# Optimization experiments

Hardware: AMD Instinct MI355X
Metric: run time of the kernel (lower is better)

## Reference

```python
import jax, jax.numpy as jnp
import numpy as np

G, N, E, C = 4, 50000, 800000, 128


def setup_inputs() -> dict:
    key = jax.random.key(0)
    ks = jax.random.split(key, 8)
    x = jax.random.normal(ks[0], (G, N, C), dtype=jnp.float32)
    edge_index = jax.random.randint(ks[1], (G, 2, E), 0, N, dtype=jnp.int64)
    s = 1.0 / np.sqrt(C)
    W1 = jax.random.normal(ks[2], (G, C, C), dtype=jnp.float32) * s
    W2 = jax.random.normal(ks[3], (G, C, C), dtype=jnp.float32) * s
    W3 = jax.random.normal(ks[4], (G, C, C), dtype=jnp.float32) * s
    b1 = jnp.zeros((G, C), dtype=jnp.float32)
    b2 = jnp.zeros((G, C), dtype=jnp.float32)
    b3 = jnp.zeros((G, C), dtype=jnp.float32)
    return {"x": x, "edge_index": edge_index, "W1": W1, "b1": b1,
            "W2": W2, "b2": b2, "W3": W3, "b3": b3}


def _gcn_layer(x, src, dst, deg_inv_sqrt, W, b):
    # PyG GCNConv: linear, then D^-1/2 (A+I) D^-1/2 aggregation, then bias.
    h = x @ W                                   # [N, C_out]
    norm = deg_inv_sqrt[src] * deg_inv_sqrt[dst]  # [E+N]
    msg = h[src] * norm[:, None]                # gather + scale
    out = jax.ops.segment_sum(msg, dst, num_segments=x.shape[0])
    return out + b


def _forward_one(x, ei, W1, b1, W2, b2, W3, b3):
    n = x.shape[0]
    loops = jnp.arange(n, dtype=ei.dtype)
    src = jnp.concatenate([ei[0], loops])       # add self-loops
    dst = jnp.concatenate([ei[1], loops])
    deg = jax.ops.segment_sum(jnp.ones_like(src, dtype=x.dtype), dst, num_segments=n)
    dis = jnp.where(deg > 0, jax.lax.rsqrt(deg), 0.0)
    x = _gcn_layer(x, src, dst, dis, W1, b1)
    x = _gcn_layer(x, src, dst, dis, W2, b2)
    x = _gcn_layer(x, src, dst, dis, W3, b3)
    return x


def reference(x, edge_index, W1, b1, W2, b2, W3, b3):
    # vmap over the num_graphs independent GCN stacks, then concat node dim
    out = jax.vmap(_forward_one)(x, edge_index, W1, b1, W2, b2, W3, b3)
    return out.reshape(-1, out.shape[-1])       # [G*N, out_channels]
```

## Files before the change

kernel.cpp:

```cpp
#include <hip/hip_runtime.h>

#define NG 4
#define NN 50000
#define NE 800000
#define NC 128
#define NB 196
#define NBT (NG * NB)
#define CAPB 48
#define LBS (NB + 1)
#define CAPQ 4608

typedef _Float16 half8 __attribute__((ext_vector_type(8)));
typedef _Float16 half4 __attribute__((ext_vector_type(4)));
typedef float f32x4 __attribute__((ext_vector_type(4)));

__global__ __launch_bounds__(256) void init_cursors(int* __restrict__ bktCur) {
  int i = blockIdx.x * blockDim.x + threadIdx.x;
  if (i < NBT) bktCur[i] = i * CAPQ;
}

__global__ __launch_bounds__(256) void bucket_scatter(
    const int* __restrict__ ei, int* __restrict__ bktCur,
    unsigned int* __restrict__ rec) {
  __shared__ int lcnt[NB];
  __shared__ int lbase[NB];
  __shared__ unsigned int lbin[CAPB * LBS];
  int g = blockIdx.y;
  int tid = threadIdx.x;
  for (int i = tid; i < NB; i += 256) lcnt[i] = 0;
  __syncthreads();
  const int* srcp = ei + (size_t)g * 2 * NE;
  const int* dstp = srcp + NE;
  int e0 = blockIdx.x * 4096;
  for (int t = tid; t < 4096; t += 256) {
    int e = e0 + t;
    if (e < NE) {
      int s = srcp[e], d = dstp[e];
      int b = d >> 8;
      unsigned int r = ((unsigned int)(d & 255) << 16) | (unsigned int)s;
      int pos = atomicAdd(&lcnt[b], 1);
      if (pos < CAPB) lbin[pos * LBS + b] = r;
      else { int gp = atomicAdd(&bktCur[g * NB + b], 1); rec[gp] = r; }
    }
  }
  __syncthreads();
  if (tid < NB) {
    int n = lcnt[tid]; if (n > CAPB) n = CAPB;
    lbase[tid] = n ? atomicAdd(&bktCur[g * NB + tid], n) : 0;
  }
  __syncthreads();
  int lane = tid & 63, wv = tid >> 6;
  for (int b = wv; b < NB; b += 4) {
    int n = lcnt[b]; if (n > CAPB) n = CAPB;
    if (lane < n) rec[lbase[b] + lane] = lbin[lane * LBS + b];
  }
}

__global__ __launch_bounds__(256) void build_csr(
    const unsigned int* __restrict__ rec, const int* __restrict__ bktCur,
    unsigned short* __restrict__ col, int* __restrict__ off,
    unsigned short* __restrict__ deg, float* __restrict__ dis) {
  __shared__ int cnt[256];
  __shared__ int offv[256];
  __shared__ int cnt2[256];
  __shared__ int wsum[4];
  int g = blockIdx.y, b = blockIdx.x;
  int idx = g * NB + b;
  int rb = idx * CAPQ, re = bktCur[idx];
  int tid = threadIdx.x;
  cnt[tid] = 0;
  __syncthreads();
  for (int j = rb + tid; j < re; j += 256)
    atomicAdd(&cnt[(rec[j] >> 16) & 255], 1);
  __syncthreads();
  int lane = tid & 63, wv = tid >> 6;
  int v = cnt[tid], incl = v;
  #pragma unroll
  for (int d2 = 1; d2 < 64; d2 <<= 1) {
    int t = __shfl_up(incl, d2, 64);
    if (lane >= d2) incl += t;
  }
  if (lane == 63) wsum[wv] = incl;
  __syncthreads();
  if (tid == 0) {
    int s = 0;
    #pragma unroll
    for (int w = 0; w < 4; ++w) { int t = wsum[w]; wsum[w] = s; s += t; }
  }
  __syncthreads();
  int excl = wsum[wv] + incl - v;
  offv[tid] = excl;
  cnt2[tid] = 0;
  int node = b * 256 + tid;
  if (node < NN) {
    off[g * (NN + 1) + node] = rb + excl;
    deg[(size_t)g * NN + node] = (unsigned short)v;
    dis[(size_t)g * NN + node] = rsqrtf((float)(v + 1));
  }
  __syncthreads();
  for (int j = rb + tid; j < re; j += 256) {
    unsigned int r = rec[j];
    int dl = (r >> 16) & 255;
    int p = rb + offv[dl] + atomicAdd(&cnt2[dl], 1);
    col[p] = (unsigned short)(r & 0xFFFF);
  }
}

__global__ __launch_bounds__(256) void gemm_mfma_kernel(
    const float* __restrict__ x, const float* __restrict__ W,
    const float* __restrict__ dis, _Float16* __restrict__ h) {
  __shared__ _Float16 Wt[2][128 * 128];
  int g = blockIdx.y;
  int row0 = blockIdx.x * 128;
  int tid = threadIdx.x;
  int lane = tid & 63;
  int wv = tid >> 6;
  int kc = lane >> 4;
  int lr = lane & 15;
  const float* Wg = W + (size_t)g * NC * NC;
  const float* xg = x + (size_t)g * NN * NC;

  {
    int n = tid & 127;
    int kq = (tid >> 7) & 1;
    #pragma unroll
    for (int iter = 0; iter < 16; ++iter) {
      int k4 = iter * 8 + kq * 4;
      float w0 = Wg[(size_t)(k4 + 0) * NC + n];
      float w1 = Wg[(size_t)(k4 + 1) * NC + n];
      float w2 = Wg[(size_t)(k4 + 2) * NC + n];
      float w3 = Wg[(size_t)(k4 + 3) * NC + n];
      half4 hi, lo;
      hi[0] = (_Float16)w0; lo[0] = (_Float16)(w0 - (float)hi[0]);
      hi[1] = (_Float16)w1; lo[1] = (_Float16)(w1 - (float)hi[1]);
      hi[2] = (_Float16)w2; lo[2] = (_Float16)(w2 - (float)hi[2]);
      hi[3] = (_Float16)w3; lo[3] = (_Float16)(w3 - (float)hi[3]);
      int base = n * 128 + ((iter ^ (n & 15)) << 3) + kq * 4;
      *(half4*)&Wt[0][base] = hi;
      *(half4*)&Wt[1][base] = lo;
    }
  }
  __syncthreads();

  f32x4 acc[2][8];
  #pragma unroll
  for (int mb = 0; mb < 2; ++mb)
    #pragma unroll
    for (int nb = 0; nb < 8; ++nb)
      acc[mb][nb] = (f32x4){0.f, 0.f, 0.f, 0.f};

  for (int kstep = 0; kstep < 4; ++kstep) {
    half8 ah[2], al[2];
    #pragma unroll
    for (int mb = 0; mb < 2; ++mb) {
      int row = row0 + wv * 32 + mb * 16 + lr;
      if (row > NN - 1) row = NN - 1;
      const float* xp = xg + (size_t)row * NC + kstep * 32 + kc * 8;
      float4 v0 = *(const float4*)xp;
      float4 v1 = *(const float4*)(xp + 4);
      float vv0 = v0.x, vv1 = v0.y, vv2 = v0.z, vv3 = v0.w;
      float vv4 = v1.x, vv5 = v1.y, vv6 = v1.z, vv7 = v1.w;
      _Float16 t;
      t = (_Float16)vv0; ah[mb][0] = t; al[mb][0] = (_Float16)(vv0 - (float)t);
      t = (_Float16)vv1; ah[mb][1] = t; al[mb][1] = (_Float16)(vv1 - (float)t);
      t = (_Float16)vv2; ah[mb][2] = t; al[mb][2] = (_Float16)(vv2 - (float)t);
      t = (_Float16)vv3; ah[mb][3] = t; al[mb][3] = (_Float16)(vv3 - (float)t);
      t = (_Float16)vv4; ah[mb][4] = t; al[mb][4] = (_Float16)(vv4 - (float)t);
      t = (_Float16)vv5; ah[mb][5] = t; al[mb][5] = (_Float16)(vv5 - (float)t);
      t = (_Float16)vv6; ah[mb][6] = t; al[mb][6] = (_Float16)(vv6 - (float)t);
      t = (_Float16)vv7; ah[mb][7] = t; al[mb][7] = (_Float16)(vv7 - (float)t);
    }
    #pragma unroll
    for (int nb = 0; nb < 8; ++nb) {
      int n = nb * 16 + lr;
      int chunk = kstep * 4 + kc;
      int boff = n * 128 + ((chunk ^ (n & 15)) << 3);
      half8 bh = *(const half8*)&Wt[0][boff];
      half8 bl = *(const half8*)&Wt[1][boff];
      #pragma unroll
      for (int mb = 0; mb < 2; ++mb) {
        acc[mb][nb] = __builtin_amdgcn_mfma_f32_16x16x32_f16(ah[mb], bh, acc[mb][nb], 0, 0, 0);
        acc[mb][nb] = __builtin_amdgcn_mfma_f32_16x16x32_f16(al[mb], bh, acc[mb][nb], 0, 0, 0);
        acc[mb][nb] = __builtin_amdgcn_mfma_f32_16x16x32_f16(ah[mb], bl, acc[mb][nb], 0, 0, 0);
      }
    }
  }

  const float* disg = dis + (size_t)g * NN;
  _Float16* hg = h + (size_t)g * NN * NC;
  #pragma unroll
  for (int mb = 0; mb < 2; ++mb) {
    #pragma unroll
    for (int reg = 0; reg < 4; ++reg) {
      int row = row0 + wv * 32 + mb * 16 + kc * 4 + reg;
      if (row < NN) {
        float dsc = disg[row];
        half8 o;
        #pragma unroll
        for (int nb = 0; nb < 8; ++nb)
          o[nb] = (_Float16)(acc[mb][nb][reg] * dsc);
        *(half8*)(hg + (size_t)row * NC + lr * 8) = o;
      }
    }
  }
}

__global__ __launch_bounds__(256) void gemm16_mfma_kernel(
    const _Float16* __restrict__ x, const float* __restrict__ W,
    const float* __restrict__ dis, _Float16* __restrict__ h) {
  __shared__ _Float16 Wt[2][128 * 128];
  int g = blockIdx.y;
  int row0 = blockIdx.x * 128;
  int tid = threadIdx.x;
  int lane = tid & 63;
  int wv = tid >> 6;
  int kc = lane >> 4;
  int lr = lane & 15;
  const float* Wg = W + (size_t)g * NC * NC;
  const _Float16* xg = x + (size_t)g * NN * NC;

  {
    int n = tid & 127;
    int kq = (tid >> 7) & 1;
    #pragma unroll
    for (int iter = 0; iter < 16; ++iter) {
      int k4 = iter * 8 + kq * 4;
      float w0 = Wg[(size_t)(k4 + 0) * NC + n];
      float w1 = Wg[(size_t)(k4 + 1) * NC + n];
      float w2 = Wg[(size_t)(k4 + 2) * NC + n];
      float w3 = Wg[(size_t)(k4 + 3) * NC + n];
      half4 hi, lo;
      hi[0] = (_Float16)w0; lo[0] = (_Float16)(w0 - (float)hi[0]);
      hi[1] = (_Float16)w1; lo[1] = (_Float16)(w1 - (float)hi[1]);
      hi[2] = (_Float16)w2; lo[2] = (_Float16)(w2 - (float)hi[2]);
      hi[3] = (_Float16)w3; lo[3] = (_Float16)(w3 - (float)hi[3]);
      int base = n * 128 + ((iter ^ (n & 15)) << 3) + kq * 4;
      *(half4*)&Wt[0][base] = hi;
      *(half4*)&Wt[1][base] = lo;
    }
  }
  __syncthreads();

  f32x4 acc[2][8];
  #pragma unroll
  for (int mb = 0; mb < 2; ++mb)
    #pragma unroll
    for (int nb = 0; nb < 8; ++nb)
      acc[mb][nb] = (f32x4){0.f, 0.f, 0.f, 0.f};

  for (int kstep = 0; kstep < 4; ++kstep) {
    half8 ah[2];
    #pragma unroll
    for (int mb = 0; mb < 2; ++mb) {
      int row = row0 + wv * 32 + mb * 16 + lr;
      if (row > NN - 1) row = NN - 1;
      ah[mb] = *(const half8*)(xg + (size_t)row * NC + kstep * 32 + kc * 8);
    }
    #pragma unroll
    for (int nb = 0; nb < 8; ++nb) {
      int n = nb * 16 + lr;
      int chunk = kstep * 4 + kc;
      int boff = n * 128 + ((chunk ^ (n & 15)) << 3);
      half8 bh = *(const half8*)&Wt[0][boff];
      half8 bl = *(const half8*)&Wt[1][boff];
      #pragma unroll
      for (int mb = 0; mb < 2; ++mb) {
        acc[mb][nb] = __builtin_amdgcn_mfma_f32_16x16x32_f16(ah[mb], bh, acc[mb][nb], 0, 0, 0);
        acc[mb][nb] = __builtin_amdgcn_mfma_f32_16x16x32_f16(ah[mb], bl, acc[mb][nb], 0, 0, 0);
      }
    }
  }

  const float* disg = dis + (size_t)g * NN;
  _Float16* hg = h + (size_t)g * NN * NC;
  #pragma unroll
  for (int mb = 0; mb < 2; ++mb) {
    #pragma unroll
    for (int reg = 0; reg < 4; ++reg) {
      int row = row0 + wv * 32 + mb * 16 + kc * 4 + reg;
      if (row < NN) {
        float dsc = disg[row];
        half8 o;
        #pragma unroll
        for (int nb = 0; nb < 8; ++nb)
          o[nb] = (_Float16)(acc[mb][nb][reg] * dsc);
        *(half8*)(hg + (size_t)row * NC + lr * 8) = o;
      }
    }
  }
}

#define MIXACC(A, H) A = fmaf((float)(H), 1.0f, A)
template <bool F16OUT>
__global__ __launch_bounds__(256) void agg_kernel(
    const _Float16* __restrict__ h, const int* __restrict__ off,
    const unsigned short* __restrict__ col, const unsigned short* __restrict__ deg,
    const float* __restrict__ dis, const float* __restrict__ b,
    float* __restrict__ outf, _Float16* __restrict__ outh) {
  int bid = blockIdx.x;
  int g = (bid & 7) >> 1;
  int sub = ((bid >> 3) << 1) | (bid & 1);
  int node = sub * 16 + (threadIdx.x >> 4);
  if (sub >= NN / 16) return;
  int l = threadIdx.x & 15;
  const half8* h8 = (const half8*)(h + (size_t)g * NN * NC);
  float a0[8], a1[8], a2[8], a3[8];
  half8 v = h8[(size_t)node * 16 + l];
  #pragma unroll
  for (int i = 0; i < 8; ++i) {
    a0[i] = (float)v[i]; a1[i] = 0.f; a2[i] = 0.f; a3[i] = 0.f;
  }
  int s = off[g * (NN + 1) + node];
  int e = s + deg[(size_t)g * NN + node];
  int j = s;
  for (; j + 4 <= e; j += 4) {
    int c0 = col[j], c1 = col[j + 1], c2 = col[j + 2], c3 = col[j + 3];
    half8 v0 = h8[(size_t)c0 * 16 + l];
    half8 v1 = h8[(size_t)c1 * 16 + l];
    half8 v2 = h8[(size_t)c2 * 16 + l];
    half8 v3 = h8[(size_t)c3 * 16 + l];
    #pragma unroll
    for (int i = 0; i < 8; ++i) {
      MIXACC(a0[i], v0[i]); MIXACC(a1[i], v1[i]);
      MIXACC(a2[i], v2[i]); MIXACC(a3[i], v3[i]);
    }
  }
  for (; j < e; ++j) {
    half8 vr = h8[(size_t)col[j] * 16 + l];
    #pragma unroll
    for (int i = 0; i < 8; ++i) MIXACC(a0[i], vr[i]);
  }
  float dn = dis[g * NN + node];
  const float* bg = b + (size_t)g * NC;
  if constexpr (F16OUT) {
    _Float16* og = outh + ((size_t)g * NN + node) * NC;
    #pragma unroll
    for (int i = 0; i < 8; ++i) {
      float val = (a0[i] + a1[i] + a2[i] + a3[i]) * dn + bg[i * 16 + l];
      og[i * 16 + l] = (_Float16)val;
    }
  } else {
    float* og = outf + ((size_t)g * NN + node) * NC;
    #pragma unroll
    for (int i = 0; i < 8; ++i) {
      float val = (a0[i] + a1[i] + a2[i] + a3[i]) * dn + bg[i * 16 + l];
      og[i * 16 + l] = val;
    }
  }
}

extern "C" void kernel_launch(void* const* d_in, const int* in_sizes, int n_in,
                              void* d_out, int out_size, void* d_ws, size_t ws_size,
                              hipStream_t stream) {
  const float* x  = (const float*)d_in[0];
  const int*   ei = (const int*)d_in[1];
  const float* W1 = (const float*)d_in[2];
  const float* b1 = (const float*)d_in[3];
  const float* W2 = (const float*)d_in[4];
  const float* b2 = (const float*)d_in[5];
  const float* W3 = (const float*)d_in[6];
  const float* b3 = (const float*)d_in[7];
  float* out = (float*)d_out;

  char* ws = (char*)d_ws;
  size_t p = 0;
  auto carve = [&](size_t bytes) -> char* {
    char* r = ws + p;
    p += (bytes + 255) & ~(size_t)255;
    return r;
  };
  int*            bktCur = (int*)           carve((size_t)NBT * 4);
  unsigned short* col    = (unsigned short*)carve((size_t)NBT * CAPQ * 2);
  int*            off    = (int*)           carve((size_t)NG * (NN + 1) * 4);
  unsigned short* deg    = (unsigned short*)carve((size_t)NG * NN * 2);
  float*          dis    = (float*)         carve((size_t)NG * NN * 4);
  _Float16*       hbuf   = (_Float16*)      carve((size_t)NG * NN * NC * 2);
  size_t ubytes = (size_t)NG * NN * NC * 2;
  char*           uni    = carve(ubytes);
  unsigned int*   rec    = (unsigned int*)uni;
  _Float16*       xh     = (_Float16*)uni;

  init_cursors<<<(NBT + 255) / 256, 256, 0, stream>>>(bktCur);
  bucket_scatter<<<dim3((NE + 4095) / 4096, NG), 256, 0, stream>>>(ei, bktCur, rec);
  build_csr<<<dim3(NB, NG), 256, 0, stream>>>(rec, bktCur, col, off, deg, dis);

  dim3 ggrid((NN + 127) / 128, NG);
  int  agrid = ((NN / 16 + 1) / 2) * 8;

  gemm_mfma_kernel<<<ggrid, 256, 0, stream>>>(x, W1, dis, hbuf);
  agg_kernel<true><<<agrid, 256, 0, stream>>>(hbuf, off, col, deg, dis, b1, nullptr, xh);
  gemm16_mfma_kernel<<<ggrid, 256, 0, stream>>>(xh, W2, dis, hbuf);
  agg_kernel<true><<<agrid, 256, 0, stream>>>(hbuf, off, col, deg, dis, b2, nullptr, xh);
  gemm16_mfma_kernel<<<ggrid, 256, 0, stream>>>(xh, W3, dis, hbuf);
  agg_kernel<false><<<agrid, 256, 0, stream>>>(hbuf, off, col, deg, dis, b3, out, nullptr);
}
```

Before: 459.8 us.

## Fuse first-layer GEMM with edge bucket scatter in one heterogeneous launch

The first GEMM no longer depends on the degree normalisation. It now runs in the same launch as the edge bucket scatter, with blocks split by index, so the compute-bound MFMA work overlaps the atomic-heavy scatter. The source-side deg^-1/2 scaling for layer 1 moves into the aggregation kernel as a per-neighbour gather of dis. The layer-2/3 GEMM now uses 512-thread blocks covering 256 rows. This costs extra per-edge dis loads in the first aggregation and larger blocks with 64KB of shared memory.

```diff
diff --git a/kernel.cpp b/kernel.cpp
--- a/kernel.cpp
+++ b/kernel.cpp
@@ -9,6 +9,7 @@
 #define CAPB 48
 #define LBS (NB + 1)
 #define CAPQ 4608
+#define GEMM_BLKS 784
 
 typedef _Float16 half8 __attribute__((ext_vector_type(8)));
 typedef _Float16 half4 __attribute__((ext_vector_type(4)));
@@ -19,40 +20,131 @@
   if (i < NBT) bktCur[i] = i * CAPQ;
 }
 
-__global__ __launch_bounds__(256) void bucket_scatter(
-    const int* __restrict__ ei, int* __restrict__ bktCur,
-    unsigned int* __restrict__ rec) {
-  __shared__ int lcnt[NB];
-  __shared__ int lbase[NB];
-  __shared__ unsigned int lbin[CAPB * LBS];
-  int g = blockIdx.y;
+__global__ __launch_bounds__(512) void fat_gemm1_scatter(
+    const float* __restrict__ x, const float* __restrict__ W,
+    _Float16* __restrict__ h, const int* __restrict__ ei,
+    int* __restrict__ bktCur, unsigned int* __restrict__ rec) {
+  __shared__ char smem[65536];
+  int bid = blockIdx.x;
   int tid = threadIdx.x;
-  for (int i = tid; i < NB; i += 256) lcnt[i] = 0;
-  __syncthreads();
-  const int* srcp = ei + (size_t)g * 2 * NE;
-  const int* dstp = srcp + NE;
-  int e0 = blockIdx.x * 4096;
-  for (int t = tid; t < 4096; t += 256) {
-    int e = e0 + t;
-    if (e < NE) {
-      int s = srcp[e], d = dstp[e];
-      int b = d >> 8;
-      unsigned int r = ((unsigned int)(d & 255) << 16) | (unsigned int)s;
-      int pos = atomicAdd(&lcnt[b], 1);
-      if (pos < CAPB) lbin[pos * LBS + b] = r;
-      else { int gp = atomicAdd(&bktCur[g * NB + b], 1); rec[gp] = r; }
-    }
-  }
-  __syncthreads();
-  if (tid < NB) {
-    int n = lcnt[tid]; if (n > CAPB) n = CAPB;
-    lbase[tid] = n ? atomicAdd(&bktCur[g * NB + tid], n) : 0;
-  }
-  __syncthreads();
-  int lane = tid & 63, wv = tid >> 6;
-  for (int b = wv; b < NB; b += 4) {
-    int n = lcnt[b]; if (n > CAPB) n = CAPB;
-    if (lane < n) rec[lbase[b] + lane] = lbin[lane * LBS + b];
+  if (bid < GEMM_BLKS) {
+    _Float16* Wt0 = (_Float16*)smem;
+    _Float16* Wt1 = Wt0 + 128 * 128;
+    int g = bid / 196;
+    int row0 = (bid % 196) * 256;
+    int lane = tid & 63;
+    int wv = tid >> 6;
+    int kc = lane >> 4;
+    int lr = lane & 15;
+    const float* Wg = W + (size_t)g * NC * NC;
+    const float* xg = x + (size_t)g * NN * NC;
+    {
+      int n = tid & 127;
+      int kq = (tid >> 7) & 3;
+      #pragma unroll
+      for (int it = 0; it < 8; ++it) {
+        int k4 = it * 16 + kq * 4;
+        float w0 = Wg[(size_t)(k4 + 0) * NC + n];
+        float w1 = Wg[(size_t)(k4 + 1) * NC + n];
+        float w2 = Wg[(size_t)(k4 + 2) * NC + n];
+        float w3 = Wg[(size_t)(k4 + 3) * NC + n];
+        half4 hi, lo;
+        hi[0] = (_Float16)w0; lo[0] = (_Float16)(w0 - (float)hi[0]);
+        hi[1] = (_Float16)w1; lo[1] = (_Float16)(w1 - (float)hi[1]);
+        hi[2] = (_Float16)w2; lo[2] = (_Float16)(w2 - (float)hi[2]);
+        hi[3] = (_Float16)w3; lo[3] = (_Float16)(w3 - (float)hi[3]);
+        int chunk = k4 >> 3;
+        int base = n * 128 + ((chunk ^ (n & 15)) << 3) + (k4 & 4);
+        *(half4*)&Wt0[base] = hi;
+        *(half4*)&Wt1[base] = lo;
+      }
+    }
+    __syncthreads();
+    f32x4 acc[2][8];
+    #pragma unroll
+    for (int mb = 0; mb < 2; ++mb)
+      #pragma unroll
+      for (int nb = 0; nb < 8; ++nb)
+        acc[mb][nb] = (f32x4){0.f, 0.f, 0.f, 0.f};
+    for (int kstep = 0; kstep < 4; ++kstep) {
+      half8 ah[2], al[2];
+      #pragma unroll
+      for (int mb = 0; mb < 2; ++mb) {
+        int row = row0 + wv * 32 + mb * 16 + lr;
+        if (row > NN - 1) row = NN - 1;
+        const float* xp = xg + (size_t)row * NC + kstep * 32 + kc * 8;
+        float4 v0 = *(const float4*)xp;
+        float4 v1 = *(const float4*)(xp + 4);
+        float vv[8] = {v0.x, v0.y, v0.z, v0.w, v1.x, v1.y, v1.z, v1.w};
+        #pragma unroll
+        for (int i = 0; i < 8; ++i) {
+          _Float16 t = (_Float16)vv[i];
+          ah[mb][i] = t; al[mb][i] = (_Float16)(vv[i] - (float)t);
+        }
+      }
+      #pragma unroll
+      for (int nb = 0; nb < 8; ++nb) {
+        int n = nb * 16 + lr;
+        int chunk = kstep * 4 + kc;
+        int boff = n * 128 + ((chunk ^ (n & 15)) << 3);
+        half8 bh = *(const half8*)&Wt0[boff];
+        half8 bl = *(const half8*)&Wt1[boff];
+        #pragma unroll
+        for (int mb = 0; mb < 2; ++mb) {
+          acc[mb][nb] = __builtin_amdgcn_mfma_f32_16x16x32_f16(ah[mb], bh, acc[mb][nb], 0, 0, 0);
+          acc[mb][nb] = __builtin_amdgcn_mfma_f32_16x16x32_f16(al[mb], bh, acc[mb][nb], 0, 0, 0);
+          acc[mb][nb] = __builtin_amdgcn_mfma_f32_16x16x32_f16(ah[mb], bl, acc[mb][nb], 0, 0, 0);
+        }
+      }
+    }
+    _Float16* hg = h + (size_t)g * NN * NC;
+    #pragma unroll
+    for (int mb = 0; mb < 2; ++mb) {
+      #pragma unroll
+      for (int reg = 0; reg < 4; ++reg) {
+        int row = row0 + wv * 32 + mb * 16 + kc * 4 + reg;
+        if (row < NN) {
+          half8 o;
+          #pragma unroll
+          for (int nb = 0; nb < 8; ++nb)
+            o[nb] = (_Float16)acc[mb][nb][reg];
+          *(half8*)(hg + (size_t)row * NC + lr * 8) = o;
+        }
+      }
+    }
+  } else {
+    int* lcnt = (int*)smem;
+    int* lbase = lcnt + NB;
+    unsigned int* lbin = (unsigned int*)(smem + 2048);
+    int sb = bid - GEMM_BLKS;
+    int g = sb / 196;
+    int e0 = (sb % 196) * 4096;
+    for (int i = tid; i < NB; i += 512) lcnt[i] = 0;
+    __syncthreads();
+    const int* srcp = ei + (size_t)g * 2 * NE;
+    const int* dstp = srcp + NE;
+    for (int t = tid; t < 4096; t += 512) {
+      int e = e0 + t;
+      if (e < NE) {
+        int s = srcp[e], d = dstp[e];
+        int b = d >> 8;
+        unsigned int r = ((unsigned int)(d & 255) << 16) | (unsigned int)s;
+        int pos = atomicAdd(&lcnt[b], 1);
+        if (pos < CAPB) lbin[pos * LBS + b] = r;
+        else { int gp = atomicAdd(&bktCur[g * NB + b], 1); rec[gp] = r; }
+      }
+    }
+    __syncthreads();
+    if (tid < NB) {
+      int n = lcnt[tid]; if (n > CAPB) n = CAPB;
+      lbase[tid] = n ? atomicAdd(&bktCur[g * NB + tid], n) : 0;
+    }
+    __syncthreads();
+    int lane = tid & 63, wv = tid >> 6;
+    for (int b = wv; b < NB; b += 8) {
+      int n = lcnt[b]; if (n > CAPB) n = CAPB;
+      if (lane < n) rec[lbase[b] + lane] = lbin[lane * LBS + b];
+    }
   }
 }
 
@@ -106,26 +198,25 @@
   }
 }
 
-__global__ __launch_bounds__(256) void gemm_mfma_kernel(
-    const float* __restrict__ x, const float* __restrict__ W,
+__global__ __launch_bounds__(512) void gemm16_mfma_kernel(
+    const _Float16* __restrict__ x, const float* __restrict__ W,
     const float* __restrict__ dis, _Float16* __restrict__ h) {
   __shared__ _Float16 Wt[2][128 * 128];
   int g = blockIdx.y;
-  int row0 = blockIdx.x * 128;
+  int row0 = blockIdx.x * 256;
   int tid = threadIdx.x;
   int lane = tid & 63;
   int wv = tid >> 6;
   int kc = lane >> 4;
   int lr = lane & 15;
   const float* Wg = W + (size_t)g * NC * NC;
-  const float* xg = x + (size_t)g * NN * NC;
-
+  const _Float16* xg = x + (size_t)g * NN * NC;
   {
     int n = tid & 127;
-    int kq = (tid >> 7) & 1;
-    #pragma unroll
-    for (int iter = 0; iter < 16; ++iter) {
-      int k4 = iter * 8 + kq * 4;
+    int kq = (tid >> 7) & 3;
+    #pragma unroll
+    for (int it = 0; it < 8; ++it) {
+      int k4 = it * 16 + kq * 4;
       float w0 = Wg[(size_t)(k4 + 0) * NC + n];
       float w1 = Wg[(size_t)(k4 + 1) * NC + n];
       float w2 = Wg[(size_t)(k4 + 2) * NC + n];
@@ -135,40 +226,26 @@
       hi[1] = (_Float16)w1; lo[1] = (_Float16)(w1 - (float)hi[1]);
       hi[2] = (_Float16)w2; lo[2] = (_Float16)(w2 - (float)hi[2]);
       hi[3] = (_Float16)w3; lo[3] = (_Float16)(w3 - (float)hi[3]);
-      int base = n * 128 + ((iter ^ (n & 15)) << 3) + kq * 4;
+      int chunk = k4 >> 3;
+      int base = n * 128 + ((chunk ^ (n & 15)) << 3) + (k4 & 4);
       *(half4*)&Wt[0][base] = hi;
       *(half4*)&Wt[1][base] = lo;
     }
   }
   __syncthreads();
-
   f32x4 acc[2][8];
   #pragma unroll
   for (int mb = 0; mb < 2; ++mb)
     #pragma unroll
     for (int nb = 0; nb < 8; ++nb)
       acc[mb][nb] = (f32x4){0.f, 0.f, 0.f, 0.f};
-
   for (int kstep = 0; kstep < 4; ++kstep) {
-    half8 ah[2], al[2];
+    half8 ah[2];
     #pragma unroll
     for (int mb = 0; mb < 2; ++mb) {
       int row = row0 + wv * 32 + mb * 16 + lr;
       if (row > NN - 1) row = NN - 1;
-      const float* xp = xg + (size_t)row * NC + kstep * 32 + kc * 8;
-      float4 v0 = *(const float4*)xp;
-      float4 v1 = *(const float4*)(xp + 4);
-      float vv0 = v0.x, vv1 = v0.y, vv2 = v0.z, vv3 = v0.w;
-      float vv4 = v1.x, vv5 = v1.y, vv6 = v1.z, vv7 = v1.w;
-      _Float16 t;
-      t = (_Float16)vv0; ah[mb][0] = t; al[mb][0] = (_Float16)(vv0 - (float)t);
-      t = (_Float16)vv1; ah[mb][1] = t; al[mb][1] = (_Float16)(vv1 - (float)t);
-      t = (_Float16)vv2; ah[mb][2] = t; al[mb][2] = (_Float16)(vv2 - (float)t);
-      t = (_Float16)vv3; ah[mb][3] = t; al[mb][3] = (_Float16)(vv3 - (float)t);
-      t = (_Float16)vv4; ah[mb][4] = t; al[mb][4] = (_Float16)(vv4 - (float)t);
-      t = (_Float16)vv5; ah[mb][5] = t; al[mb][5] = (_Float16)(vv5 - (float)t);
-      t = (_Float16)vv6; ah[mb][6] = t; al[mb][6] = (_Float16)(vv6 - (float)t);
-      t = (_Float16)vv7; ah[mb][7] = t; al[mb][7] = (_Float16)(vv7 - (float)t);
+      ah[mb] = *(const half8*)(xg + (size_t)row * NC + kstep * 32 + kc * 8);
     }
     #pragma unroll
     for (int nb = 0; nb < 8; ++nb) {
@@ -180,12 +257,10 @@
       #pragma unroll
       for (int mb = 0; mb < 2; ++mb) {
         acc[mb][nb] = __builtin_amdgcn_mfma_f32_16x16x32_f16(ah[mb], bh, acc[mb][nb], 0, 0, 0);
-        acc[mb][nb] = __builtin_amdgcn_mfma_f32_16x16x32_f16(al[mb], bh, acc[mb][nb], 0, 0, 0);
         acc[mb][nb] = __builtin_amdgcn_mfma_f32_16x16x32_f16(ah[mb], bl, acc[mb][nb], 0, 0, 0);
       }
     }
   }
-
   const float* disg = dis + (size_t)g * NN;
   _Float16* hg = h + (size_t)g * NN * NC;
   #pragma unroll
@@ -205,93 +280,9 @@
   }
 }
 
-__global__ __launch_bounds__(256) void gemm16_mfma_kernel(
-    const _Float16* __restrict__ x, const float* __restrict__ W,
-    const float* __restrict__ dis, _Float16* __restrict__ h) {
-  __shared__ _Float16 Wt[2][128 * 128];
-  int g = blockIdx.y;
-  int row0 = blockIdx.x * 128;
-  int tid = threadIdx.x;
-  int lane = tid & 63;
-  int wv = tid >> 6;
-  int kc = lane >> 4;
-  int lr = lane & 15;
-  const float* Wg = W + (size_t)g * NC * NC;
-  const _Float16* xg = x + (size_t)g * NN * NC;
-
-  {
-    int n = tid & 127;
-    int kq = (tid >> 7) & 1;
-    #pragma unroll
-    for (int iter = 0; iter < 16; ++iter) {
-      int k4 = iter * 8 + kq * 4;
-      float w0 = Wg[(size_t)(k4 + 0) * NC + n];
-      float w1 = Wg[(size_t)(k4 + 1) * NC + n];
-      float w2 = Wg[(size_t)(k4 + 2) * NC + n];
-      float w3 = Wg[(size_t)(k4 + 3) * NC + n];
-      half4 hi, lo;
-      hi[0] = (_Float16)w0; lo[0] = (_Float16)(w0 - (float)hi[0]);
-      hi[1] = (_Float16)w1; lo[1] = (_Float16)(w1 - (float)hi[1]);
-      hi[2] = (_Float16)w2; lo[2] = (_Float16)(w2 - (float)hi[2]);
-      hi[3] = (_Float16)w3; lo[3] = (_Float16)(w3 - (float)hi[3]);
-      int base = n * 128 + ((iter ^ (n & 15)) << 3) + kq * 4;
-      *(half4*)&Wt[0][base] = hi;
-      *(half4*)&Wt[1][base] = lo;
-    }
-  }
-  __syncthreads();
-
-  f32x4 acc[2][8];
-  #pragma unroll
-  for (int mb = 0; mb < 2; ++mb)
-    #pragma unroll
-    for (int nb = 0; nb < 8; ++nb)
-      acc[mb][nb] = (f32x4){0.f, 0.f, 0.f, 0.f};
-
-  for (int kstep = 0; kstep < 4; ++kstep) {
-    half8 ah[2];
-    #pragma unroll
-    for (int mb = 0; mb < 2; ++mb) {
-      int row = row0 + wv * 32 + mb * 16 + lr;
-      if (row > NN - 1) row = NN - 1;
-      ah[mb] = *(const half8*)(xg + (size_t)row * NC + kstep * 32 + kc * 8);
-    }
-    #pragma unroll
-    for (int nb = 0; nb < 8; ++nb) {
-      int n = nb * 16 + lr;
-      int chunk = kstep * 4 + kc;
-      int boff = n * 128 + ((chunk ^ (n & 15)) << 3);
-      half8 bh = *(const half8*)&Wt[0][boff];
-      half8 bl = *(const half8*)&Wt[1][boff];
-      #pragma unroll
-      for (int mb = 0; mb < 2; ++mb) {
-        acc[mb][nb] = __builtin_amdgcn_mfma_f32_16x16x32_f16(ah[mb], bh, acc[mb][nb], 0, 0, 0);
-        acc[mb][nb] = __builtin_amdgcn_mfma_f32_16x16x32_f16(ah[mb], bl, acc[mb][nb], 0, 0, 0);
-      }
-    }
-  }
-
-  const float* disg = dis + (size_t)g * NN;
-  _Float16* hg = h + (size_t)g * NN * NC;
-  #pragma unroll
-  for (int mb = 0; mb < 2; ++mb) {
-    #pragma unroll
-    for (int reg = 0; reg < 4; ++reg) {
-      int row = row0 + wv * 32 + mb * 16 + kc * 4 + reg;
-      if (row < NN) {
-        float dsc = disg[row];
-        half8 o;
-        #pragma unroll
-        for (int nb = 0; nb < 8; ++nb)
-          o[nb] = (_Float16)(acc[mb][nb][reg] * dsc);
-        *(half8*)(hg + (size_t)row * NC + lr * 8) = o;
-      }
-    }
-  }
-}
-
 #define MIXACC(A, H) A = fmaf((float)(H), 1.0f, A)
-template <bool F16OUT>
+#define MIXS(A, H, S) A = fmaf((float)(H), S, A)
+template <bool F16OUT, bool GDIS>
 __global__ __launch_bounds__(256) void agg_kernel(
     const _Float16* __restrict__ h, const int* __restrict__ off,
     const unsigned short* __restrict__ col, const unsigned short* __restrict__ deg,
@@ -304,11 +295,14 @@
   if (sub >= NN / 16) return;
   int l = threadIdx.x & 15;
   const half8* h8 = (const half8*)(h + (size_t)g * NN * NC);
+  const float* disg = dis + (size_t)g * NN;
+  float dn = disg[node];
   float a0[8], a1[8], a2[8], a3[8];
   half8 v = h8[(size_t)node * 16 + l];
   #pragma unroll
   for (int i = 0; i < 8; ++i) {
-    a0[i] = (float)v[i]; a1[i] = 0.f; a2[i] = 0.f; a3[i] = 0.f;
+    a0[i] = GDIS ? dn * (float)v[i] : (float)v[i];
+    a1[i] = 0.f; a2[i] = 0.f; a3[i] = 0.f;
   }
   int s = off[g * (NN + 1) + node];
   int e = s + deg[(size_t)g * NN + node];
@@ -319,18 +313,33 @@
     half8 v1 = h8[(size_t)c1 * 16 + l];
     half8 v2 = h8[(size_t)c2 * 16 + l];
     half8 v3 = h8[(size_t)c3 * 16 + l];
-    #pragma unroll
-    for (int i = 0; i < 8; ++i) {
-      MIXACC(a0[i], v0[i]); MIXACC(a1[i], v1[i]);
-      MIXACC(a2[i], v2[i]); MIXACC(a3[i], v3[i]);
+    if constexpr (GDIS) {
+      float d0 = disg[c0], d1 = disg[c1], d2 = disg[c2], d3 = disg[c3];
+      #pragma unroll
+      for (int i = 0; i < 8; ++i) {
+        MIXS(a0[i], v0[i], d0); MIXS(a1[i], v1[i], d1);
+        MIXS(a2[i], v2[i], d2); MIXS(a3[i], v3[i], d3);
+      }
+    } else {
+      #pragma unroll
+      for (int i = 0; i < 8; ++i) {
+        MIXACC(a0[i], v0[i]); MIXACC(a1[i], v1[i]);
+        MIXACC(a2[i], v2[i]); MIXACC(a3[i], v3[i]);
+      }
     }
   }
   for (; j < e; ++j) {
-    half8 vr = h8[(size_t)col[j] * 16 + l];
-    #pragma unroll
-    for (int i = 0; i < 8; ++i) MIXACC(a0[i], vr[i]);
-  }
-  float dn = dis[g * NN + node];
+    int c = col[j];
+    half8 vr = h8[(size_t)c * 16 + l];
+    if constexpr (GDIS) {
+      float dd = disg[c];
+      #pragma unroll
+      for (int i = 0; i < 8; ++i) MIXS(a0[i], vr[i], dd);
+    } else {
+      #pragma unroll
+      for (int i = 0; i < 8; ++i) MIXACC(a0[i], vr[i]);
+    }
+  }
   const float* bg = b + (size_t)g * NC;
   if constexpr (F16OUT) {
     _Float16* og = outh + ((size_t)g * NN + node) * NC;
@@ -381,16 +390,15 @@
   _Float16*       xh     = (_Float16*)uni;
 
   init_cursors<<<(NBT + 255) / 256, 256, 0, stream>>>(bktCur);
-  bucket_scatter<<<dim3((NE + 4095) / 4096, NG), 256, 0, stream>>>(ei, bktCur, rec);
+  fat_gemm1_scatter<<<GEMM_BLKS + 784, 512, 0, stream>>>(x, W1, hbuf, ei, bktCur, rec);
   build_csr<<<dim3(NB, NG), 256, 0, stream>>>(rec, bktCur, col, off, deg, dis);
 
-  dim3 ggrid((NN + 127) / 128, NG);
+  dim3 ggrid((NN + 255) / 256, NG);
   int  agrid = ((NN / 16 + 1) / 2) * 8;
 
-  gemm_mfma_kernel<<<ggrid, 256, 0, stream>>>(x, W1, dis, hbuf);
-  agg_kernel<true><<<agrid, 256, 0, stream>>>(hbuf, off, col, deg, dis, b1, nullptr, xh);
-  gemm16_mfma_kernel<<<ggrid, 256, 0, stream>>>(xh, W2, dis, hbuf);
-  agg_kernel<true><<<agrid, 256, 0, stream>>>(hbuf, off, col, deg, dis, b2, nullptr, xh);
-  gemm16_mfma_kernel<<<ggrid, 256, 0, stream>>>(xh, W3, dis, hbuf);
-  agg_kernel<false><<<agrid, 256, 0, stream>>>(hbuf, off, col, deg, dis, b3, out, nullptr);
-}
+  agg_kernel<true, true><<<agrid, 256, 0, stream>>>(hbuf, off, col, deg, dis, b1, nullptr, xh);
+  gemm16_mfma_kernel<<<ggrid, 512, 0, stream>>>(xh, W2, dis, hbuf);
+  agg_kernel<true, false><<<agrid, 256, 0, stream>>>(hbuf, off, col, deg, dis, b2, nullptr, xh);
+  gemm16_mfma_kernel<<<ggrid, 512, 0, stream>>>(xh, W3, dis, hbuf);
+  agg_kernel<false, false><<<agrid, 256, 0, stream>>>(hbuf, off, col, deg, dis, b3, out, nullptr);
+}
```

Measured after the change: 443.4 us, median of 2. 1.04x faster.
